# Kernel tuning notes

Measured on AMD Instinct MI355X. Metric: run time of the kernel, lower is better.

The kernel has to match this reference:

```python
import jax, jax.numpy as jnp
import numpy as np

B, C, L = 8, 2048, 256          # batch, seq (EEG channels), feature length
E = 3 * L                        # embed_dim = 768 (fused QKV width)
H = 4                            # attention heads
D = E // (3 * H)                 # head_dim = 64
SCALE = 8.0                      # hardcoded in the module (== sqrt(D) here)


def _layer_norm(x, gamma, beta, eps=1e-5):
    mu = jnp.mean(x, axis=-1, keepdims=True)
    var = jnp.var(x, axis=-1, keepdims=True)
    return (x - mu) * jax.lax.rsqrt(var + eps) * gamma + beta


def setup_inputs() -> dict:
    key = jax.random.key(0)
    ks = jax.random.split(key, 5)
    x = jax.random.normal(ks[0], (B, C, L), dtype=jnp.float32)
    # layers_1: Linear(L -> E) + LayerNorm(E)
    W1 = jax.random.normal(ks[1], (L, E), dtype=jnp.float32) / np.sqrt(L)
    b1 = jnp.zeros((E,), dtype=jnp.float32)
    g1 = jnp.ones((E,), dtype=jnp.float32)
    beta1 = jnp.zeros((E,), dtype=jnp.float32)
    # layers_2: Linear(L -> L) + LayerNorm(L)
    W2 = jax.random.normal(ks[2], (L, L), dtype=jnp.float32) / np.sqrt(L)
    b2 = jnp.zeros((L,), dtype=jnp.float32)
    g2 = jnp.ones((L,), dtype=jnp.float32)
    beta2 = jnp.zeros((L,), dtype=jnp.float32)
    return {"x": x, "W1": W1, "b1": b1, "g1": g1, "beta1": beta1,
            "W2": W2, "b2": b2, "g2": g2, "beta2": beta2}


def reference(x, W1, b1, g1, beta1, W2, b2, g2, beta2):
    b, c, _ = x.shape
    # layers_1 (dropout is identity in eval mode)
    y = _layer_norm(x @ W1 + b1, g1, beta1)                     # [b, c, E]
    qkv = y.reshape(b, c, 3, H, D).transpose(2, 0, 3, 1, 4)     # [3, b, H, c, D]
    q, k, v = qkv[0], qkv[1], qkv[2]
    attn = jax.nn.softmax(jnp.einsum('bhqd,bhkd->bhqk', q, k) / SCALE, axis=-1)
    o = jnp.einsum('bhqk,bhkd->bhqd', attn, v)                  # [b, H, c, D]
    o = o.transpose(0, 2, 1, 3).reshape(b, c, H * D)            # [b, c, L]
    # layers_2 + residual
    z = _layer_norm(o @ W2 + b2, g2, beta2) + x
    return z
```

## Files before the change

kernel.cpp:

```cpp
#include <hip/hip_runtime.h>
#include <hip/hip_bf16.h>

#define B_ 8
#define C_ 2048
#define L_ 256
#define E_ 768
#define H_ 4
#define D_ 64
#define M_ (B_*C_)

typedef __attribute__((ext_vector_type(8))) short short8v;
typedef __attribute__((ext_vector_type(4))) short short4v;
typedef __attribute__((ext_vector_type(4))) float f32x4;

__device__ __forceinline__ short f2bf(float f) {
  union { float f; unsigned u; } v; v.f = f;
  unsigned r = v.u + 0x7FFFu + ((v.u >> 16) & 1u);
  return (short)(r >> 16);
}
__device__ __forceinline__ unsigned cvtpk(float a, float b) {
  unsigned r;
  asm("v_cvt_pk_bf16_f32 %0, %1, %2" : "=v"(r) : "v"(a), "v"(b));
  return r;
}
__device__ __forceinline__ float exp2x(float x) {
  float r;
  asm("v_exp_f32 %0, %1" : "=v"(r) : "v"(x));
  return r;
}

__device__ __forceinline__ void gll16(const void* g, void* l) {
  __builtin_amdgcn_global_load_lds(
      (const __attribute__((address_space(1))) unsigned int*)g,
      (__attribute__((address_space(3))) unsigned int*)l, 16, 0, 0);
}

__global__ __launch_bounds__(256) void transpose_w_kernel(const float* __restrict__ W,
                                                          short* __restrict__ Wt,
                                                          int K, int N) {
  __shared__ float ld[32][33];
  const int k0 = blockIdx.x * 32, n0 = blockIdx.y * 32;
  const int tx = threadIdx.x & 31, ty = threadIdx.x >> 5;
  #pragma unroll
  for (int j = 0; j < 4; ++j)
    ld[ty + j*8][tx] = W[(size_t)(k0 + ty + j*8) * N + n0 + tx];
  __syncthreads();
  const int r  = threadIdx.x >> 3;
  const int c0 = (threadIdx.x & 7) * 4;
  short4v o;
  o[0]=f2bf(ld[c0+0][r]); o[1]=f2bf(ld[c0+1][r]);
  o[2]=f2bf(ld[c0+2][r]); o[3]=f2bf(ld[c0+3][r]);
  *(short4v*)(Wt + (size_t)(n0 + r) * K + k0 + c0) = o;
}

__global__ __launch_bounds__(512, 2) void gemm1_ln_fused_kernel(
    const float* __restrict__ x, const short* __restrict__ W1t,
    const float* __restrict__ b1, const float* __restrict__ g1,
    const float* __restrict__ be1,
    short* __restrict__ Qg, short* __restrict__ Kg, short* __restrict__ Vtg) {
  __shared__ short As[32*264];
  __shared__ float2 red[8][32];
  __shared__ float mu_s[32], rs_s[32];
  const int tid = threadIdx.x;
  const int w = tid >> 6, l = tid & 63, lo = l & 15, hi = l >> 4;
  const int m0 = blockIdx.x * 32;
  const int b = m0 >> 11, c0 = m0 & (C_ - 1);
  const int nbase = w * 96;

  {
    const int row = tid >> 4, cc = (tid & 15) * 16;
    const float* ap = x + (size_t)(m0 + row) * 256 + cc;
    float4 a0 = ((const float4*)ap)[0], a1 = ((const float4*)ap)[1];
    float4 a2 = ((const float4*)ap)[2], a3 = ((const float4*)ap)[3];
    uint4 p0, p1;
    p0.x = cvtpk(a0.x,a0.y); p0.y = cvtpk(a0.z,a0.w);
    p0.z = cvtpk(a1.x,a1.y); p0.w = cvtpk(a1.z,a1.w);
    p1.x = cvtpk(a2.x,a2.y); p1.y = cvtpk(a2.z,a2.w);
    p1.z = cvtpk(a3.x,a3.y); p1.w = cvtpk(a3.z,a3.w);
    *(uint4*)&As[row*264 + cc]     = p0;
    *(uint4*)&As[row*264 + cc + 8] = p1;
  }
  __syncthreads();

  f32x4 acc[2][6];
  #pragma unroll
  for (int m = 0; m < 2; ++m)
    #pragma unroll
    for (int n = 0; n < 6; ++n) acc[m][n] = (f32x4){0.f,0.f,0.f,0.f};

  #pragma unroll
  for (int kt = 0; kt < 4; ++kt)
    #pragma unroll
    for (int kk = 0; kk < 2; ++kk) {
      short8v bf[6];
      #pragma unroll
      for (int n = 0; n < 6; ++n)
        bf[n] = *(const short8v*)(W1t + (size_t)(nbase + n*16 + lo) * 256
                                     + kt*64 + kk*32 + hi*8);
      short8v af0 = *(short8v*)&As[lo*264      + kt*64 + kk*32 + hi*8];
      short8v af1 = *(short8v*)&As[(16+lo)*264 + kt*64 + kk*32 + hi*8];
      #pragma unroll
      for (int n = 0; n < 6; ++n) {
        acc[0][n] = __builtin_amdgcn_mfma_f32_16x16x32_bf16(af0, bf[n], acc[0][n], 0,0,0);
        acc[1][n] = __builtin_amdgcn_mfma_f32_16x16x32_bf16(af1, bf[n], acc[1][n], 0,0,0);
      }
    }

  float bb[6], ggv[6], eev[6];
  #pragma unroll
  for (int n = 0; n < 6; ++n) {
    int col = nbase + n*16 + lo;
    bb[n] = b1[col]; ggv[n] = g1[col]; eev[n] = be1[col];
  }
  #pragma unroll
  for (int m = 0; m < 2; ++m)
    #pragma unroll
    for (int r = 0; r < 4; ++r) {
      float s = 0.f, s2 = 0.f;
      #pragma unroll
      for (int n = 0; n < 6; ++n) {
        float v = acc[m][n][r] + bb[n];
        acc[m][n][r] = v;
        s += v; s2 += v*v;
      }
      #pragma unroll
      for (int off = 1; off < 16; off <<= 1) {
        s  += __shfl_xor(s, off);
        s2 += __shfl_xor(s2, off);
      }
      if (lo == 0) red[w][m*16 + hi*4 + r] = make_float2(s, s2);
    }
  __syncthreads();
  if (tid < 32) {
    float s = 0.f, s2 = 0.f;
    #pragma unroll
    for (int wv = 0; wv < 8; ++wv) { s += red[wv][tid].x; s2 += red[wv][tid].y; }
    float mu = s * (1.f / E_);
    float var = s2 * (1.f / E_) - mu * mu;
    mu_s[tid] = mu;
    rs_s[tid] = rsqrtf(var + 1e-5f);
  }
  __syncthreads();

  const float qs = 0.18033688011f;
  #pragma unroll
  for (int m = 0; m < 2; ++m) {
    float mu4[4], rs4[4];
    #pragma unroll
    for (int r = 0; r < 4; ++r) {
      int row = m*16 + hi*4 + r;
      mu4[r] = mu_s[row]; rs4[r] = rs_s[row];
    }
    const int cbase = c0 + m*16 + hi*4;
    #pragma unroll
    for (int n = 0; n < 6; ++n) {
      const int e0 = nbase + n*16 + lo;
      float vals[4];
      #pragma unroll
      for (int r = 0; r < 4; ++r)
        vals[r] = (acc[m][n][r] - mu4[r]) * rs4[r] * ggv[n] + eev[n];
      if (e0 < 256) {
        const int h = e0 >> 6, d = e0 & 63;
        short* base = Qg + ((size_t)(b*H_ + h) * C_) * D_ + d;
        #pragma unroll
        for (int r = 0; r < 4; ++r)
          base[(size_t)(cbase + r) * D_] = f2bf(vals[r] * qs);
      } else if (e0 < 512) {
        const int eb = e0 - 256, h = eb >> 6, d = eb & 63;
        short* base = Kg + ((size_t)(b*H_ + h) * C_) * D_;
        #pragma unroll
        for (int r = 0; r < 4; ++r) {
          int c = cbase + r;
          base[(size_t)c * D_ + (((d>>3) ^ (c&7)) << 3) + (d&7)] = f2bf(vals[r]);
        }
      } else {
        const int eb = e0 - 512, h = eb >> 6, d = eb & 63;
        short4v pk;
        #pragma unroll
        for (int r = 0; r < 4; ++r) pk[r] = f2bf(vals[r]);
        const int c = cbase;
        size_t off = ((size_t)(b*H_ + h) * D_ + d) * C_ + (c & ~63)
                   + ((((c & 63) >> 3) ^ (d & 7)) << 3) + (c & 7);
        *(short4v*)(Vtg + off) = pk;
      }
    }
  }
}

__global__ __launch_bounds__(512, 4) void attn_mfma_kernel(
    const short* __restrict__ Qg, const short* __restrict__ Kg,
    const short* __restrict__ Vtg, short* __restrict__ ob) {
  __shared__ short Ks[3][4096];
  __shared__ short Vs[3][4096];
  __shared__ short Ps[8][1024];
  const int tid = threadIdx.x;
  const int w  = tid >> 6;
  const int l  = tid & 63, lo = l & 15, hi = l >> 4;
  const int sw = lo & 7;
  const int bh = blockIdx.x, qt = blockIdx.y;
  const size_t hd = (size_t)bh * (C_ * D_);
  const int q0 = qt * 128 + w * 16;

  const short8v bq0 = *(const short8v*)(Qg + hd + (size_t)(q0+lo)*D_ + hi*8);
  const short8v bq1 = *(const short8v*)(Qg + hd + (size_t)(q0+lo)*D_ + 32 + hi*8);

  short8v ones;
  #pragma unroll
  for (int j = 0; j < 8; ++j) ones[j] = (short)0x3F80;

  const short* Ktile = Kg + hd;
  const short* Vrow  = Vtg + hd;
  const int kOff = w*512 + l*8;
  const size_t vOff = (size_t)(w*8 + (l>>3)) * C_ + (l&7)*8;

  f32x4 Oacc[4] = {{0,0,0,0},{0,0,0,0},{0,0,0,0},{0,0,0,0}};
  f32x4 Lacc = {0.f, 0.f, 0.f, 0.f};
  const f32x4 zero4 = {0.f, 0.f, 0.f, 0.f};
  short* Pw = &Ps[w][0];

  gll16(Ktile + kOff, &Ks[0][w*512]);
  gll16(Vrow + vOff,  &Vs[0][w*512]);

  int cur = 0, nxt = 1;
  for (int kt = 0; kt < 32; ++kt) {
    asm volatile("s_waitcnt vmcnt(0)" ::: "memory");
    __builtin_amdgcn_s_barrier();
    if (kt != 31) {
      const short* kn = Ktile + (size_t)(kt+1) * 4096;
      const short* vn = Vrow  + (size_t)(kt+1) * 64;
      gll16(kn + kOff, &Ks[nxt][w*512]);
      gll16(vn + vOff, &Vs[nxt][w*512]);
    }
    const short* Kc = &Ks[cur][0];
    const short* Vc = &Vs[cur][0];

    f32x4 st[4];
    __builtin_amdgcn_s_setprio(1);
    #pragma unroll
    for (int mt = 0; mt < 4; ++mt) {
      short8v ka = *(const short8v*)&Kc[(mt*16 + lo)*64 + ((hi ^ sw) << 3)];
      short8v kb = *(const short8v*)&Kc[(mt*16 + lo)*64 + (((4 + hi) ^ sw) << 3)];
      f32x4 z = __builtin_amdgcn_mfma_f32_16x16x32_bf16(ka, bq0, zero4, 0, 0, 0);
      st[mt]  = __builtin_amdgcn_mfma_f32_16x16x32_bf16(kb, bq1, z, 0, 0, 0);
    }
    __builtin_amdgcn_s_setprio(0);

    float ps[16];
    #pragma unroll
    for (int mt = 0; mt < 4; ++mt)
      #pragma unroll
      for (int r = 0; r < 4; ++r)
        ps[mt*4 + r] = exp2x(st[mt][r]);

    #pragma unroll
    for (int mt = 0; mt < 4; ++mt) {
      uint2 pk;
      pk.x = cvtpk(ps[mt*4+0], ps[mt*4+1]);
      pk.y = cvtpk(ps[mt*4+2], ps[mt*4+3]);
      *(uint2*)&Pw[lo*64 + ((((mt<<1) + (hi>>1)) ^ sw) << 3) + ((hi&1) << 2)] = pk;
    }
    asm volatile("s_waitcnt lgkmcnt(0)" ::: "memory");

    short8v pa0 = *(short8v*)&Pw[lo*64 + ((hi ^ sw) << 3)];
    short8v pa1 = *(short8v*)&Pw[lo*64 + (((4 + hi) ^ sw) << 3)];
    __builtin_amdgcn_s_setprio(1);
    Lacc = __builtin_amdgcn_mfma_f32_16x16x32_bf16(pa0, ones, Lacc, 0, 0, 0);
    Lacc = __builtin_amdgcn_mfma_f32_16x16x32_bf16(pa1, ones, Lacc, 0, 0, 0);
    #pragma unroll
    for (int nt = 0; nt < 4; ++nt) {
      short8v vb0 = *(const short8v*)&Vc[(nt*16 + lo)*64 + ((hi ^ sw) << 3)];
      short8v vb1 = *(const short8v*)&Vc[(nt*16 + lo)*64 + (((4 + hi) ^ sw) << 3)];
      Oacc[nt] = __builtin_amdgcn_mfma_f32_16x16x32_bf16(pa0, vb0, Oacc[nt], 0,0,0);
      Oacc[nt] = __builtin_amdgcn_mfma_f32_16x16x32_bf16(pa1, vb1, Oacc[nt], 0,0,0);
    }
    __builtin_amdgcn_s_setprio(0);
    cur = nxt;
    nxt = (nxt == 2) ? 0 : nxt + 1;
  }

  float invL[4];
  #pragma unroll
  for (int r = 0; r < 4; ++r) invL[r] = 1.f / Lacc[r];
  const int b = bh >> 2, h = bh & 3;
  short* obp = ob + ((size_t)b * C_ + q0) * L_ + h * D_;
  #pragma unroll
  for (int nt = 0; nt < 4; ++nt)
    #pragma unroll
    for (int r = 0; r < 4; ++r)
      obp[(hi*4 + r) * L_ + nt*16 + lo] = f2bf(Oacc[nt][r] * invL[r]);
}

__global__ __launch_bounds__(256) void gemm2_ln_mfma_kernel(
    const short* __restrict__ ob, const short* __restrict__ W2t,
    const float* __restrict__ b2, const float* __restrict__ g2,
    const float* __restrict__ be2, const float* __restrict__ x,
    float* __restrict__ out) {
  __shared__ short As[64*72];
  __shared__ short Bs[256*72];
  __shared__ float2 red[2][2][32];
  const int tid = threadIdx.x;
  const int w = tid >> 6, l = tid & 63, lo = l & 15, hi = l >> 4;
  const int wr = w >> 1, wc = w & 1;
  const int m0 = blockIdx.x * 64;

  f32x4 acc[2][8];
  #pragma unroll
  for (int m = 0; m < 2; ++m)
    #pragma unroll
    for (int n = 0; n < 8; ++n) acc[m][n] = (f32x4){0.f,0.f,0.f,0.f};

  for (int kt = 0; kt < 4; ++kt) {
    __syncthreads();
    #pragma unroll
    for (int i = 0; i < 2; ++i) {
      int id = tid + i * 256;
      int row = id >> 3, k8 = (id & 7) * 8;
      *(short8v*)&As[row*72 + k8] =
          *(const short8v*)(ob + (size_t)(m0 + row) * 256 + kt*64 + k8);
    }
    #pragma unroll
    for (int i = 0; i < 8; ++i) {
      int id = tid + i * 256;
      int row = id >> 3, k8 = (id & 7) * 8;
      *(short8v*)&Bs[row*72 + k8] =
          *(const short8v*)(W2t + (size_t)row * 256 + kt*64 + k8);
    }
    __syncthreads();
    #pragma unroll
    for (int kk = 0; kk < 2; ++kk) {
      short8v af[2], bf[8];
      #pragma unroll
      for (int m = 0; m < 2; ++m)
        af[m] = *(short8v*)&As[(wr*32 + m*16 + lo)*72 + kk*32 + hi*8];
      #pragma unroll
      for (int n = 0; n < 8; ++n)
        bf[n] = *(short8v*)&Bs[(wc*128 + n*16 + lo)*72 + kk*32 + hi*8];
      #pragma unroll
      for (int m = 0; m < 2; ++m)
        #pragma unroll
        for (int n = 0; n < 8; ++n)
          acc[m][n] = __builtin_amdgcn_mfma_f32_16x16x32_bf16(af[m], bf[n], acc[m][n], 0,0,0);
    }
  }

  float bb[8], gg[8], ee[8];
  #pragma unroll
  for (int n = 0; n < 8; ++n) {
    int col = wc*128 + n*16 + lo;
    bb[n] = b2[col]; gg[n] = g2[col]; ee[n] = be2[col];
  }
  float ps[2][4], pq[2][4];
  #pragma unroll
  for (int m = 0; m < 2; ++m)
    #pragma unroll
    for (int r = 0; r < 4; ++r) {
      float s = 0.f, s2 = 0.f;
      #pragma unroll
      for (int n = 0; n < 8; ++n) {
        float v = acc[m][n][r] + bb[n];
        acc[m][n][r] = v;
        s += v; s2 += v*v;
      }
      ps[m][r] = s; pq[m][r] = s2;
    }
  #pragma unroll
  for (int off = 1; off < 16; off <<= 1)
    #pragma unroll
    for (int m = 0; m < 2; ++m)
      #pragma unroll
      for (int r = 0; r < 4; ++r) {
        ps[m][r] += __shfl_xor(ps[m][r], off);
        pq[m][r] += __shfl_xor(pq[m][r], off);
      }
  if (lo == 0)
    #pragma unroll
    for (int m = 0; m < 2; ++m)
      #pragma unroll
      for (int r = 0; r < 4; ++r)
        red[wr][wc][m*16 + hi*4 + r] = make_float2(ps[m][r], pq[m][r]);
  __syncthreads();

  #pragma unroll
  for (int m = 0; m < 2; ++m)
    #pragma unroll
    for (int r = 0; r < 4; ++r) {
      float2 t0 = red[wr][0][m*16 + hi*4 + r];
      float2 t1 = red[wr][1][m*16 + hi*4 + r];
      float s = t0.x + t1.x, s2 = t0.y + t1.y;
      float mu  = s * (1.f / L_);
      float var = s2 * (1.f / L_) - mu * mu;
      float rs  = rsqrtf(var + 1e-5f);
      const int grow = m0 + wr*32 + m*16 + hi*4 + r;
      const float* xr = x + (size_t)grow * L_ + wc*128;
      float* orow = out + (size_t)grow * L_ + wc*128;
      #pragma unroll
      for (int n = 0; n < 8; ++n)
        orow[n*16 + lo] = (acc[m][n][r] - mu) * rs * gg[n] + ee[n] + xr[n*16 + lo];
    }
}

extern "C" void kernel_launch(void* const* d_in, const int* in_sizes, int n_in,
                              void* d_out, int out_size, void* d_ws, size_t ws_size,
                              hipStream_t stream) {
  const float* x   = (const float*)d_in[0];
  const float* W1  = (const float*)d_in[1];
  const float* b1  = (const float*)d_in[2];
  const float* g1  = (const float*)d_in[3];
  const float* be1 = (const float*)d_in[4];
  const float* W2  = (const float*)d_in[5];
  const float* b2  = (const float*)d_in[6];
  const float* g2  = (const float*)d_in[7];
  const float* be2 = (const float*)d_in[8];
  float* out = (float*)d_out;

  const size_t HDSZ = (size_t)B_ * H_ * C_ * D_;
  short* W1t = (short*)d_ws;
  short* W2t = W1t + (size_t)L_ * E_;
  short* Qg  = W2t + (size_t)L_ * L_;
  short* Kg  = Qg  + HDSZ;
  short* Vtg = Kg  + HDSZ;
  short* obm = Vtg + HDSZ;

  transpose_w_kernel<<<dim3(8, 24), 256, 0, stream>>>(W1, W1t, L_, E_);
  transpose_w_kernel<<<dim3(8, 8),  256, 0, stream>>>(W2, W2t, L_, L_);
  gemm1_ln_fused_kernel<<<M_ / 32, 512, 0, stream>>>(x, W1t, b1, g1, be1, Qg, Kg, Vtg);
  attn_mfma_kernel<<<dim3(32, C_ / 128), 512, 0, stream>>>(Qg, Kg, Vtg, obm);
  gemm2_ln_mfma_kernel<<<M_ / 64, 256, 0, stream>>>(obm, W2t, b2, g2, be2, x, out);
}
```

Baseline: 102.8 us.

## Merge weight transposes into one launch and restructure gemm2 to stream W2 from global

The two weight-transpose launches are merged into a single grid that branches on blockIdx.y, removing one kernel launch. gemm2 now uses 32-row tiles, with the whole A tile staged once in LDS. Each wave owns 64 output columns and reads its W2 fragments straight from global/L2 instead of staging B in LDS with a K loop and barriers. The grid is doubled and a launch-bounds hint is added for higher occupancy. The LayerNorm reduction moves to a per-block shared-memory pass. The trade-off is that W2 is re-read from cache by every block, with no LDS reuse.

After: 103.6 us. No clear change (+0.8%).

```diff
diff --git a/kernel.cpp b/kernel.cpp
--- a/kernel.cpp
+++ b/kernel.cpp
@@ -35,11 +35,15 @@
       (__attribute__((address_space(3))) unsigned int*)l, 16, 0, 0);
 }
 
-__global__ __launch_bounds__(256) void transpose_w_kernel(const float* __restrict__ W,
-                                                          short* __restrict__ Wt,
-                                                          int K, int N) {
+__global__ __launch_bounds__(256) void transpose_w_kernel(
+    const float* __restrict__ W1, short* __restrict__ W1t,
+    const float* __restrict__ W2, short* __restrict__ W2t) {
   __shared__ float ld[32][33];
-  const int k0 = blockIdx.x * 32, n0 = blockIdx.y * 32;
+  const int isW1 = blockIdx.y < 24;
+  const float* W = isW1 ? W1 : W2;
+  short* Wt = isW1 ? W1t : W2t;
+  const int N = isW1 ? E_ : L_;
+  const int k0 = blockIdx.x * 32, n0 = (isW1 ? blockIdx.y : blockIdx.y - 24) * 32;
   const int tx = threadIdx.x & 31, ty = threadIdx.x >> 5;
   #pragma unroll
   for (int j = 0; j < 4; ++j)
@@ -50,7 +54,7 @@
   short4v o;
   o[0]=f2bf(ld[c0+0][r]); o[1]=f2bf(ld[c0+1][r]);
   o[2]=f2bf(ld[c0+2][r]); o[3]=f2bf(ld[c0+3][r]);
-  *(short4v*)(Wt + (size_t)(n0 + r) * K + k0 + c0) = o;
+  *(short4v*)(Wt + (size_t)(n0 + r) * 256 + k0 + c0) = o;
 }
 
 __global__ __launch_bounds__(512, 2) void gemm1_ln_fused_kernel(
@@ -290,113 +294,107 @@
       obp[(hi*4 + r) * L_ + nt*16 + lo] = f2bf(Oacc[nt][r] * invL[r]);
 }
 
-__global__ __launch_bounds__(256) void gemm2_ln_mfma_kernel(
+__global__ __launch_bounds__(256, 4) void gemm2_ln_mfma_kernel(
     const short* __restrict__ ob, const short* __restrict__ W2t,
     const float* __restrict__ b2, const float* __restrict__ g2,
     const float* __restrict__ be2, const float* __restrict__ x,
     float* __restrict__ out) {
-  __shared__ short As[64*72];
-  __shared__ short Bs[256*72];
-  __shared__ float2 red[2][2][32];
+  __shared__ short As[32*264];
+  __shared__ float2 red[4][32];
+  __shared__ float mu_s[32], rs_s[32];
   const int tid = threadIdx.x;
   const int w = tid >> 6, l = tid & 63, lo = l & 15, hi = l >> 4;
-  const int wr = w >> 1, wc = w & 1;
-  const int m0 = blockIdx.x * 64;
-
-  f32x4 acc[2][8];
+  const int m0 = blockIdx.x * 32;
+  const int nbase = w * 64;
+
+  #pragma unroll
+  for (int i = 0; i < 4; ++i) {
+    int id = tid + i * 256;
+    int row = id >> 5, c8 = (id & 31) * 8;
+    *(short8v*)&As[row*264 + c8] =
+        *(const short8v*)(ob + (size_t)(m0 + row) * 256 + c8);
+  }
+  __syncthreads();
+
+  f32x4 acc[2][4];
   #pragma unroll
   for (int m = 0; m < 2; ++m)
     #pragma unroll
-    for (int n = 0; n < 8; ++n) acc[m][n] = (f32x4){0.f,0.f,0.f,0.f};
-
-  for (int kt = 0; kt < 4; ++kt) {
-    __syncthreads();
-    #pragma unroll
-    for (int i = 0; i < 2; ++i) {
-      int id = tid + i * 256;
-      int row = id >> 3, k8 = (id & 7) * 8;
-      *(short8v*)&As[row*72 + k8] =
-          *(const short8v*)(ob + (size_t)(m0 + row) * 256 + kt*64 + k8);
-    }
-    #pragma unroll
-    for (int i = 0; i < 8; ++i) {
-      int id = tid + i * 256;
-      int row = id >> 3, k8 = (id & 7) * 8;
-      *(short8v*)&Bs[row*72 + k8] =
-          *(const short8v*)(W2t + (size_t)row * 256 + kt*64 + k8);
-    }
-    __syncthreads();
+    for (int n = 0; n < 4; ++n) acc[m][n] = (f32x4){0.f,0.f,0.f,0.f};
+
+  #pragma unroll
+  for (int kt = 0; kt < 4; ++kt)
     #pragma unroll
     for (int kk = 0; kk < 2; ++kk) {
-      short8v af[2], bf[8];
-      #pragma unroll
-      for (int m = 0; m < 2; ++m)
-        af[m] = *(short8v*)&As[(wr*32 + m*16 + lo)*72 + kk*32 + hi*8];
-      #pragma unroll
-      for (int n = 0; n < 8; ++n)
-        bf[n] = *(short8v*)&Bs[(wc*128 + n*16 + lo)*72 + kk*32 + hi*8];
-      #pragma unroll
-      for (int m = 0; m < 2; ++m)
-        #pragma unroll
-        for (int n = 0; n < 8; ++n)
-          acc[m][n] = __builtin_amdgcn_mfma_f32_16x16x32_bf16(af[m], bf[n], acc[m][n], 0,0,0);
-    }
-  }
-
-  float bb[8], gg[8], ee[8];
-  #pragma unroll
-  for (int n = 0; n < 8; ++n) {
-    int col = wc*128 + n*16 + lo;
+      short8v bf[4];
+      #pragma unroll
+      for (int n = 0; n < 4; ++n)
+        bf[n] = *(const short8v*)(W2t + (size_t)(nbase + n*16 + lo) * 256
+                                     + kt*64 + kk*32 + hi*8);
+      short8v af0 = *(short8v*)&As[lo*264      + kt*64 + kk*32 + hi*8];
+      short8v af1 = *(short8v*)&As[(16+lo)*264 + kt*64 + kk*32 + hi*8];
+      #pragma unroll
+      for (int n = 0; n < 4; ++n) {
+        acc[0][n] = __builtin_amdgcn_mfma_f32_16x16x32_bf16(af0, bf[n], acc[0][n], 0,0,0);
+        acc[1][n] = __builtin_amdgcn_mfma_f32_16x16x32_bf16(af1, bf[n], acc[1][n], 0,0,0);
+      }
+    }
+
+  float bb[4], gg[4], ee[4];
+  #pragma unroll
+  for (int n = 0; n < 4; ++n) {
+    int col = nbase + n*16 + lo;
     bb[n] = b2[col]; gg[n] = g2[col]; ee[n] = be2[col];
   }
-  float ps[2][4], pq[2][4];
   #pragma unroll
   for (int m = 0; m < 2; ++m)
     #pragma unroll
     for (int r = 0; r < 4; ++r) {
       float s = 0.f, s2 = 0.f;
       #pragma unroll
-      for (int n = 0; n < 8; ++n) {
+      for (int n = 0; n < 4; ++n) {
         float v = acc[m][n][r] + bb[n];
         acc[m][n][r] = v;
         s += v; s2 += v*v;
       }
-      ps[m][r] = s; pq[m][r] = s2;
-    }
-  #pragma unroll
-  for (int off = 1; off < 16; off <<= 1)
-    #pragma unroll
-    for (int m = 0; m < 2; ++m)
-      #pragma unroll
-      for (int r = 0; r < 4; ++r) {
-        ps[m][r] += __shfl_xor(ps[m][r], off);
-        pq[m][r] += __shfl_xor(pq[m][r], off);
-      }
-  if (lo == 0)
-    #pragma unroll
-    for (int m = 0; m < 2; ++m)
-      #pragma unroll
-      for (int r = 0; r < 4; ++r)
-        red[wr][wc][m*16 + hi*4 + r] = make_float2(ps[m][r], pq[m][r]);
-  __syncthreads();
-
-  #pragma unroll
-  for (int m = 0; m < 2; ++m)
+      #pragma unroll
+      for (int off = 1; off < 16; off <<= 1) {
+        s  += __shfl_xor(s, off);
+        s2 += __shfl_xor(s2, off);
+      }
+      if (lo == 0) red[w][m*16 + hi*4 + r] = make_float2(s, s2);
+    }
+  __syncthreads();
+  if (tid < 32) {
+    float s = 0.f, s2 = 0.f;
+    #pragma unroll
+    for (int wv = 0; wv < 4; ++wv) { s += red[wv][tid].x; s2 += red[wv][tid].y; }
+    float mu = s * (1.f / L_);
+    float var = s2 * (1.f / L_) - mu * mu;
+    mu_s[tid] = mu;
+    rs_s[tid] = rsqrtf(var + 1e-5f);
+  }
+  __syncthreads();
+
+  #pragma unroll
+  for (int m = 0; m < 2; ++m) {
+    float mu4[4], rs4[4];
     #pragma unroll
     for (int r = 0; r < 4; ++r) {
-      float2 t0 = red[wr][0][m*16 + hi*4 + r];
-      float2 t1 = red[wr][1][m*16 + hi*4 + r];
-      float s = t0.x + t1.x, s2 = t0.y + t1.y;
-      float mu  = s * (1.f / L_);
-      float var = s2 * (1.f / L_) - mu * mu;
-      float rs  = rsqrtf(var + 1e-5f);
-      const int grow = m0 + wr*32 + m*16 + hi*4 + r;
-      const float* xr = x + (size_t)grow * L_ + wc*128;
-      float* orow = out + (size_t)grow * L_ + wc*128;
-      #pragma unroll
-      for (int n = 0; n < 8; ++n)
-        orow[n*16 + lo] = (acc[m][n][r] - mu) * rs * gg[n] + ee[n] + xr[n*16 + lo];
-    }
+      int row = m*16 + hi*4 + r;
+      mu4[r] = mu_s[row]; rs4[r] = rs_s[row];
+    }
+    #pragma unroll
+    for (int r = 0; r < 4; ++r) {
+      const int grow = m0 + m*16 + hi*4 + r;
+      const float* xr = x + (size_t)grow * L_ + nbase;
+      float* orow = out + (size_t)grow * L_ + nbase;
+      #pragma unroll
+      for (int n = 0; n < 4; ++n)
+        orow[n*16 + lo] = (acc[m][n][r] - mu4[r]) * rs4[r] * gg[n] + ee[n]
+                        + xr[n*16 + lo];
+    }
+  }
 }
 
 extern "C" void kernel_launch(void* const* d_in, const int* in_sizes, int n_in,
@@ -421,9 +419,8 @@
   short* Vtg = Kg  + HDSZ;
   short* obm = Vtg + HDSZ;
 
-  transpose_w_kernel<<<dim3(8, 24), 256, 0, stream>>>(W1, W1t, L_, E_);
-  transpose_w_kernel<<<dim3(8, 8),  256, 0, stream>>>(W2, W2t, L_, L_);
+  transpose_w_kernel<<<dim3(8, 32), 256, 0, stream>>>(W1, W1t, W2, W2t);
   gemm1_ln_fused_kernel<<<M_ / 32, 512, 0, stream>>>(x, W1t, b1, g1, be1, Qg, Kg, Vtg);
   attn_mfma_kernel<<<dim3(32, C_ / 128), 512, 0, stream>>>(Qg, Kg, Vtg, obm);
-  gemm2_ln_mfma_kernel<<<M_ / 64, 256, 0, stream>>>(obm, W2t, b2, g2, be2, x, out);
-}
+  gemm2_ln_mfma_kernel<<<M_ / 32, 256, 0, stream>>>(obm, W2t, b2, g2, be2, x, out);
+}
```
